# Kernel optimization log

Measured on AMD Instinct MI355X. Metric: run time of the kernel, lower is better.

The kernel has to match this reference:

```python
import jax, jax.numpy as jnp
import numpy as np

B, S, H = 8, 2048, 512
M = 4096
TEMP = 0.1
EPS = 1e-6


def setup_inputs() -> dict:
    key = jax.random.key(0)
    ks = jax.random.split(key, 8)
    scale = 1.0 / np.sqrt(H)
    return {
        "hidden_states": jax.random.normal(ks[0], (B, S, H), dtype=jnp.float32),
        "memory_keys": jax.random.normal(ks[1], (M, H), dtype=jnp.float32),
        "memory_values": jax.random.normal(ks[2], (M, H), dtype=jnp.float32),
        "Wk": jax.random.normal(ks[3], (H, H), dtype=jnp.float32) * scale,
        "bk": jnp.zeros((H,), dtype=jnp.float32),
        "Wo": jax.random.normal(ks[4], (H, H), dtype=jnp.float32) * scale,
        "bo": jnp.zeros((H,), dtype=jnp.float32),
        "memory_usage": jax.random.randint(ks[5], (M,), 0, 2, dtype=jnp.int32),
    }


def reference(hidden_states, memory_keys, memory_values, Wk, bk, Wo, bo, memory_usage):
    # key projection: [B,S,H]
    q = jnp.einsum("bsh,kh->bsk", hidden_states, Wk) + bk
    # L2-style normalization with eps inside rsqrt (matches torch.rsqrt(norm_sq + 1e-6))
    q_n = q * jax.lax.rsqrt(jnp.sum(q * q, axis=-1, keepdims=True) + EPS)
    mk_n = memory_keys * jax.lax.rsqrt(
        jnp.sum(memory_keys * memory_keys, axis=-1, keepdims=True) + EPS
    )
    # cosine-similarity scores over the memory bank: [B,S,M]
    scores = jnp.einsum("bsk,mk->bsm", q_n, mk_n) / TEMP
    mask = (memory_usage > 0).astype(scores.dtype)  # [M]
    scores = scores * mask + (-1e9) * (1.0 - mask)
    attn = jax.nn.softmax(scores, axis=-1)  # [B,S,M]
    retrieved = jnp.einsum("bsm,mv->bsv", attn, memory_values)  # [B,S,H]
    out = jnp.einsum("bsv,hv->bsh", retrieved, Wo) + bo
    return out
```

## Files before the change

### kernel.cpp

```cpp
#include <hip/hip_runtime.h>
#include <cstdint>
#include <cstddef>

#define H_DIM   512
#define M_DIM   4096

typedef unsigned short u16;
typedef short bf16x8 __attribute__((ext_vector_type(8)));
typedef float f32x4  __attribute__((ext_vector_type(4)));

__device__ __forceinline__ u16 f2b(float f) {
  union { float f; uint32_t u; } v; v.f = f;
  uint32_t u = v.u + (0x7FFFu + ((v.u >> 16) & 1u));
  return (u16)(u >> 16);
}

__global__ void k_f2bf(const float* __restrict__ in, u16* __restrict__ out, int n4) {
  int i = blockIdx.x * blockDim.x + threadIdx.x;
  if (i < n4) {
    float4 v = ((const float4*)in)[i];
    ushort4 o;
    o.x = f2b(v.x); o.y = f2b(v.y); o.z = f2b(v.z); o.w = f2b(v.w);
    ((ushort4*)out)[i] = o;
  }
}

__global__ void k_f2bf_ww(const float* __restrict__ wk, const float* __restrict__ wo,
                          u16* __restrict__ owk, u16* __restrict__ owo) {
  int i = blockIdx.x * blockDim.x + threadIdx.x;
  const float* src = (i < 65536) ? wk : wo;
  u16* dst = (i < 65536) ? owk : owo;
  int j = i & 65535;
  float4 v = ((const float4*)src)[j];
  ushort4 o;
  o.x = f2b(v.x); o.y = f2b(v.y); o.z = f2b(v.z); o.w = f2b(v.w);
  ((ushort4*)dst)[j] = o;
}

__global__ void k_compact(const int* __restrict__ usage, int* __restrict__ idx,
                          int* __restrict__ meta) {
  __shared__ int cnt[256];
  int t = threadIdx.x;
  int base = t * 16;
  int c = 0;
  #pragma unroll
  for (int i = 0; i < 16; ++i) c += (usage[base + i] > 0) ? 1 : 0;
  cnt[t] = c;
  __syncthreads();
  for (int d = 1; d < 256; d <<= 1) {
    int v = (t >= d) ? cnt[t - d] : 0;
    __syncthreads();
    cnt[t] += v;
    __syncthreads();
  }
  int pos = cnt[t] - c;
  for (int i = 0; i < 16; ++i)
    if (usage[base + i] > 0) idx[pos++] = base + i;
  if (t == 0) {
    int total = cnt[255];
    int keff = ((total + 127) >> 7) << 7;
    meta[0] = total; meta[1] = keff; meta[2] = keff >> 5; meta[3] = keff >> 7;
  }
}

__global__ void k_gather_both(const float* __restrict__ keys, const float* __restrict__ vals,
                              const int* __restrict__ idx, const int* __restrict__ meta,
                              u16* __restrict__ okeys, u16* __restrict__ ovals) {
  int j    = blockIdx.x * 4 + (threadIdx.x >> 6);
  int lane = threadIdx.x & 63;
  int count = meta[0];
  ushort4* kp = (ushort4*)(okeys + (size_t)j * H_DIM);
  ushort4* vp = (ushort4*)(ovals + (size_t)j * H_DIM);
  if (j >= count) {
    ushort4 z = {0, 0, 0, 0};
    kp[lane] = z; kp[lane + 64] = z;
    vp[lane] = z; vp[lane + 64] = z;
    return;
  }
  int src = idx[j];
  const float4* rp = (const float4*)(keys + (size_t)src * H_DIM);
  float4 a = rp[lane];
  float4 b = rp[lane + 64];
  float ss = a.x*a.x + a.y*a.y + a.z*a.z + a.w*a.w
           + b.x*b.x + b.y*b.y + b.z*b.z + b.w*b.w;
  #pragma unroll
  for (int d = 1; d < 64; d <<= 1) ss += __shfl_xor(ss, d, 64);
  float s = rsqrtf(ss + 1e-6f);
  ushort4 oa, ob;
  oa.x = f2b(a.x*s); oa.y = f2b(a.y*s); oa.z = f2b(a.z*s); oa.w = f2b(a.w*s);
  ob.x = f2b(b.x*s); ob.y = f2b(b.y*s); ob.z = f2b(b.z*s); ob.w = f2b(b.w*s);
  kp[lane]      = oa;
  kp[lane + 64] = ob;
  const float4* vr = (const float4*)(vals + (size_t)src * H_DIM);
  float4 c0 = vr[lane];
  float4 c1 = vr[lane + 64];
  ushort4 va, vb;
  va.x = f2b(c0.x); va.y = f2b(c0.y); va.z = f2b(c0.z); va.w = f2b(c0.w);
  vb.x = f2b(c1.x); vb.y = f2b(c1.y); vb.z = f2b(c1.z); vb.w = f2b(c1.w);
  vp[lane]      = va;
  vp[lane + 64] = vb;
}

__global__ void k_rsq(const float* __restrict__ qss, float* __restrict__ rsq) {
  int r = blockIdx.x * blockDim.x + threadIdx.x;
  float s = qss[r*4] + qss[r*4+1] + qss[r*4+2] + qss[r*4+3];
  rsq[r] = rsqrtf(s + 1e-6f);
}

__global__ void k_reduce_l(const float* __restrict__ lpart, float* __restrict__ linv,
                           const int* __restrict__ meta) {
  int r = blockIdx.x * blockDim.x + threadIdx.x;
  int n = meta[3];
  float s = 0.0f;
  for (int i = 0; i < n; ++i) s += lpart[(size_t)r * 32 + i];
  linv[r] = 1.0f / s;
}

#define EPI_QPROJ 0
#define EPI_MW    1
#define EPI_P     2
#define EPI_OUT   3

template<int EPI>
__global__ __launch_bounds__(256)
void k_gemm_bt(const u16* __restrict__ A, const u16* __restrict__ B,
               int N, int K,
               const int* __restrict__ meta,
               float* __restrict__ outf, u16* __restrict__ outh,
               const float* __restrict__ bias,
               float* __restrict__ aux,
               const float* __restrict__ rowscale) {
  __shared__ u16 Ah[2][128 * 32];
  __shared__ u16 Bh[2][128 * 32];
  __shared__ float lsh[128];

  const int tid  = threadIdx.x;
  const int wave = tid >> 6, lane = tid & 63;
  const int wr = (wave >> 1) * 64;
  const int wc = (wave & 1) * 64;

  int rb, cb0, cb_end, cb_step, kel;
  if (EPI == EPI_QPROJ) {
    rb = blockIdx.y; cb0 = blockIdx.x; cb_end = cb0 + 1; cb_step = 1; kel = K;
  } else if (EPI == EPI_MW) {
    rb = blockIdx.y; cb0 = blockIdx.x; cb_end = meta[1] >> 7; cb_step = 16; kel = K;
  } else if (EPI == EPI_P) {
    int id = blockIdx.x + (blockIdx.y << 4);
    int xcd = id & 7, s = id >> 3;
    rb = xcd * 16 + (s >> 4); cb0 = s & 15;
    cb_end = meta[1] >> 7; cb_step = 16; kel = K;
  } else {
    int id = blockIdx.x + (blockIdx.y << 2);
    int xcd = id & 7, s = id >> 3;
    rb = xcd * 16 + (s >> 2); cb0 = s & 3;
    cb_end = cb0 + 1; cb_step = 1; kel = meta[1];
  }
  const int row0 = rb << 7;
  const int kiters = kel >> 5;

  const int srow   = lane & 15;
  const int schunk = lane >> 4;
  const int lds_off = schunk * 128 + srow * 8;
  size_t aBase[2];
  #pragma unroll
  for (int s2 = 0; s2 < 2; ++s2)
    aBase[s2] = (size_t)(row0 + (wave + s2 * 4) * 16 + srow) * (size_t)K + schunk * 8;
  size_t bBase[2];

  const int fr = lane & 15;
  const int fbase = (lane >> 4) * 128 + fr * 8;

  for (int cb = cb0; cb < cb_end; cb += cb_step) {
    const int col0 = cb << 7;
    __syncthreads();
    if ((EPI == EPI_QPROJ || EPI == EPI_P) && tid < 128) lsh[tid] = 0.0f;

    #pragma unroll
    for (int s2 = 0; s2 < 2; ++s2)
      bBase[s2] = (size_t)(col0 + (wave + s2 * 4) * 16 + srow) * (size_t)K + schunk * 8;

    f32x4 acc[4][4];
    const f32x4 z = {0.0f, 0.0f, 0.0f, 0.0f};
    #pragma unroll
    for (int i = 0; i < 4; ++i)
      #pragma unroll
      for (int j = 0; j < 4; ++j) acc[i][j] = z;

    bf16x8 rA[2], rB[2];
    auto gload = [&](int k0) {
      #pragma unroll
      for (int s2 = 0; s2 < 2; ++s2) rA[s2] = *(const bf16x8*)(A + aBase[s2] + k0);
      #pragma unroll
      for (int s2 = 0; s2 < 2; ++s2) rB[s2] = *(const bf16x8*)(B + bBase[s2] + k0);
    };

    gload(0);
    for (int it = 0; it < kiters; ++it) {
      const int cur = it & 1;
      #pragma unroll
      for (int s2 = 0; s2 < 2; ++s2)
        *(bf16x8*)&Ah[cur][(wave + s2 * 4) * 512 + lds_off] = rA[s2];
      #pragma unroll
      for (int s2 = 0; s2 < 2; ++s2)
        *(bf16x8*)&Bh[cur][(wave + s2 * 4) * 512 + lds_off] = rB[s2];
      if (it + 1 < kiters) gload((it + 1) << 5);
      __syncthreads();

      bf16x8 af[4], bfv[4];
      #pragma unroll
      for (int i = 0; i < 4; ++i)
        af[i] = *(const bf16x8*)&Ah[cur][((wr >> 4) + i) * 512 + fbase];
      #pragma unroll
      for (int j = 0; j < 4; ++j)
        bfv[j] = *(const bf16x8*)&Bh[cur][((wc >> 4) + j) * 512 + fbase];
      #pragma unroll
      for (int i = 0; i < 4; ++i)
        #pragma unroll
        for (int j = 0; j < 4; ++j)
          acc[i][j] = __builtin_amdgcn_mfma_f32_16x16x32_bf16(af[i], bfv[j], acc[i][j], 0, 0, 0);
    }

    if (EPI == EPI_QPROJ) {
      float bv[4];
      #pragma unroll
      for (int j = 0; j < 4; ++j) bv[j] = bias[col0 + wc + j * 16 + fr];
      #pragma unroll
      for (int i = 0; i < 4; ++i) {
        #pragma unroll
        for (int r = 0; r < 4; ++r) {
          int lrow = wr + i * 16 + (lane >> 4) * 4 + r;
          size_t grow = (size_t)(row0 + lrow);
          float s = 0.0f;
          #pragma unroll
          for (int j = 0; j < 4; ++j) {
            int gcol = col0 + wc + j * 16 + fr;
            float v = acc[i][j][r] + bv[j];
            outh[grow * (size_t)N + gcol] = f2b(v);
            s += v * v;
          }
          #pragma unroll
          for (int d = 1; d < 16; d <<= 1) s += __shfl_xor(s, d, 64);
          if (fr == 0) atomicAdd(&lsh[lrow], s);
        }
      }
      __syncthreads();
      if (tid < 128) aux[(size_t)(row0 + tid) * 4 + cb] = lsh[tid];
    } else if (EPI == EPI_MW) {
      #pragma unroll
      for (int i = 0; i < 4; ++i) {
        #pragma unroll
        for (int r = 0; r < 4; ++r) {
          int grow = row0 + wr + i * 16 + (lane >> 4) * 4 + r;
          #pragma unroll
          for (int j = 0; j < 4; ++j) {
            int gcol = col0 + wc + j * 16 + fr;
            outh[(size_t)grow * (size_t)N + gcol] = f2b(acc[i][j][r]);
          }
        }
      }
    } else if (EPI == EPI_P) {
      const int count = meta[0];
      #pragma unroll
      for (int i = 0; i < 4; ++i) {
        #pragma unroll
        for (int r = 0; r < 4; ++r) {
          int lrow = wr + i * 16 + (lane >> 4) * 4 + r;
          size_t grow = (size_t)(row0 + lrow);
          float rq10 = rowscale[grow] * 10.0f;
          float s = 0.0f;
          #pragma unroll
          for (int j = 0; j < 4; ++j) {
            int gcol = col0 + wc + j * 16 + fr;
            float p = (gcol < count) ? __expf(acc[i][j][r] * rq10) : 0.0f;
            outh[grow * (size_t)N + gcol] = f2b(p);
            s += p;
          }
          #pragma unroll
          for (int d = 1; d < 16; d <<= 1) s += __shfl_xor(s, d, 64);
          if (fr == 0) atomicAdd(&lsh[lrow], s);
        }
      }
      __syncthreads();
      if (tid < 128) aux[(size_t)(row0 + tid) * 32 + cb] = lsh[tid];
    } else {
      float bv[4];
      #pragma unroll
      for (int j = 0; j < 4; ++j) bv[j] = bias[col0 + wc + j * 16 + fr];
      #pragma unroll
      for (int i = 0; i < 4; ++i) {
        #pragma unroll
        for (int r = 0; r < 4; ++r) {
          int grow = row0 + wr + i * 16 + (lane >> 4) * 4 + r;
          float sc = rowscale[grow];
          #pragma unroll
          for (int j = 0; j < 4; ++j) {
            int gcol = col0 + wc + j * 16 + fr;
            outf[(size_t)grow * (size_t)N + gcol] = acc[i][j][r] * sc + bv[j];
          }
        }
      }
    }
  }
}

extern "C" void kernel_launch(void* const* d_in, const int* in_sizes, int n_in,
                              void* d_out, int out_size, void* d_ws, size_t ws_size,
                              hipStream_t stream) {
  const float* hidden = (const float*)d_in[0];
  const float* mkeys  = (const float*)d_in[1];
  const float* mvals  = (const float*)d_in[2];
  const float* Wk     = (const float*)d_in[3];
  const float* bk     = (const float*)d_in[4];
  const float* Wo     = (const float*)d_in[5];
  const float* bo     = (const float*)d_in[6];
  const int*   usage  = (const int*)d_in[7];
  (void)in_sizes; (void)n_in; (void)out_size; (void)ws_size;

  char* ws = (char*)d_ws;
  u16*   hb    = (u16*)(ws + 0);
  int*   idx   = (int*)(ws + 0);
  int*   meta  = (int*)(ws + 16384);
  u16*   wkb   = (u16*)(ws + 16777216);
  u16*   wob   = (u16*)(ws + 17301504);
  u16*   mkn   = (u16*)(ws + 17825792);
  u16*   mv_c  = (u16*)(ws + 22020096);
  u16*   qb    = (u16*)(ws + 26214400);
  u16*   MWt   = (u16*)(ws + 42991616);
  u16*   P     = (u16*)(ws + 47185920);
  float* qss   = (float*)(ws + 181403648);
  float* rsqQ  = (float*)(ws + 181665792);
  float* lpart = (float*)(ws + 181731328);
  float* linv  = (float*)(ws + 183828480);

  k_f2bf<<<8192, 256, 0, stream>>>(hidden, hb, 2097152);
  k_f2bf_ww<<<512, 256, 0, stream>>>(Wk, Wo, wkb, wob);

  k_gemm_bt<EPI_QPROJ><<<dim3(4, 128), 256, 0, stream>>>(hb, wkb, 512, 512,
      nullptr, nullptr, qb, bk, qss, nullptr);
  k_rsq<<<64, 256, 0, stream>>>(qss, rsqQ);

  k_compact<<<1, 256, 0, stream>>>(usage, idx, meta);
  k_gather_both<<<1024, 256, 0, stream>>>(mkeys, mvals, idx, meta, mkn, mv_c);

  k_gemm_bt<EPI_MW><<<dim3(16, 4), 256, 0, stream>>>(wob, mv_c, M_DIM, 512,
      meta, nullptr, MWt, nullptr, nullptr, nullptr);

  k_gemm_bt<EPI_P><<<dim3(16, 128), 256, 0, stream>>>(qb, mkn, M_DIM, 512,
      meta, nullptr, P, nullptr, lpart, rsqQ);
  k_reduce_l<<<64, 256, 0, stream>>>(lpart, linv, meta);

  k_gemm_bt<EPI_OUT><<<dim3(4, 128), 256, 0, stream>>>(P, MWt, 512, M_DIM,
      meta, (float*)d_out, nullptr, bo, nullptr, linv);
}
```

Before: 292.1 us.

## Swap GEMM operands so epilogues write packed ushort4 along contiguous dim

The Q-projection and score GEMMs are restructured to compute the transposed tile (memory/weight rows as M, tokens as N), so each lane's four accumulator rows map to contiguous output elements and can be stored as one 8-byte ushort4 instead of scattered 2-byte stores. Row-sum partials for normalisation and softmax are now reduced with two shuffles and written straight to global memory, removing the LDS atomics and extra block barrier. The kernel also uses 32-bit byte offsets for global loads and raises the launch-bounds occupancy hint, and workspace buffers are relocated. The risk is extra register pressure from the occupancy hint and a larger partial-sum array to reduce afterwards.

```diff
diff --git a/kernel.cpp b/kernel.cpp
--- a/kernel.cpp
+++ b/kernel.cpp
@@ -103,16 +103,18 @@
 
 __global__ void k_rsq(const float* __restrict__ qss, float* __restrict__ rsq) {
   int r = blockIdx.x * blockDim.x + threadIdx.x;
-  float s = qss[r*4] + qss[r*4+1] + qss[r*4+2] + qss[r*4+3];
+  float s = 0.0f;
+  #pragma unroll
+  for (int i = 0; i < 8; ++i) s += qss[(size_t)r * 8 + i];
   rsq[r] = rsqrtf(s + 1e-6f);
 }
 
 __global__ void k_reduce_l(const float* __restrict__ lpart, float* __restrict__ linv,
                            const int* __restrict__ meta) {
   int r = blockIdx.x * blockDim.x + threadIdx.x;
-  int n = meta[3];
+  int n = meta[1] >> 6;
   float s = 0.0f;
-  for (int i = 0; i < n; ++i) s += lpart[(size_t)r * 32 + i];
+  for (int i = 0; i < n; ++i) s += lpart[(size_t)r * 64 + i];
   linv[r] = 1.0f / s;
 }
 
@@ -122,7 +124,7 @@
 #define EPI_OUT   3
 
 template<int EPI>
-__global__ __launch_bounds__(256)
+__global__ __launch_bounds__(256, 3)
 void k_gemm_bt(const u16* __restrict__ A, const u16* __restrict__ B,
                int N, int K,
                const int* __restrict__ meta,
@@ -132,52 +134,55 @@
                const float* __restrict__ rowscale) {
   __shared__ u16 Ah[2][128 * 32];
   __shared__ u16 Bh[2][128 * 32];
-  __shared__ float lsh[128];
 
   const int tid  = threadIdx.x;
   const int wave = tid >> 6, lane = tid & 63;
   const int wr = (wave >> 1) * 64;
   const int wc = (wave & 1) * 64;
 
-  int rb, cb0, cb_end, cb_step, kel;
+  int t0, t_end, t_step, kel, fixedb;
   if (EPI == EPI_QPROJ) {
-    rb = blockIdx.y; cb0 = blockIdx.x; cb_end = cb0 + 1; cb_step = 1; kel = K;
+    fixedb = blockIdx.x; t0 = blockIdx.y; t_end = t0 + 1; t_step = 1; kel = K;
   } else if (EPI == EPI_MW) {
-    rb = blockIdx.y; cb0 = blockIdx.x; cb_end = meta[1] >> 7; cb_step = 16; kel = K;
+    fixedb = blockIdx.y; t0 = blockIdx.x; t_end = meta[1] >> 7; t_step = 16; kel = K;
   } else if (EPI == EPI_P) {
     int id = blockIdx.x + (blockIdx.y << 4);
     int xcd = id & 7, s = id >> 3;
-    rb = xcd * 16 + (s >> 4); cb0 = s & 15;
-    cb_end = meta[1] >> 7; cb_step = 16; kel = K;
+    fixedb = xcd * 16 + (s >> 4);
+    t0 = s & 15;
+    t_end = meta[1] >> 7; t_step = 16; kel = K;
   } else {
     int id = blockIdx.x + (blockIdx.y << 2);
     int xcd = id & 7, s = id >> 3;
-    rb = xcd * 16 + (s >> 2); cb0 = s & 3;
-    cb_end = cb0 + 1; cb_step = 1; kel = meta[1];
-  }
-  const int row0 = rb << 7;
+    fixedb = xcd * 16 + (s >> 2);
+    t0 = s & 3; t_end = t0 + 1; t_step = 1; kel = meta[1];
+  }
   const int kiters = kel >> 5;
 
   const int srow   = lane & 15;
   const int schunk = lane >> 4;
   const int lds_off = schunk * 128 + srow * 8;
-  size_t aBase[2];
-  #pragma unroll
-  for (int s2 = 0; s2 < 2; ++s2)
-    aBase[s2] = (size_t)(row0 + (wave + s2 * 4) * 16 + srow) * (size_t)K + schunk * 8;
-  size_t bBase[2];
 
   const int fr = lane & 15;
   const int fbase = (lane >> 4) * 128 + fr * 8;
-
-  for (int cb = cb0; cb < cb_end; cb += cb_step) {
-    const int col0 = cb << 7;
+  const int g = lane >> 4;
+
+  const char* Ac = (const char*)A;
+  const char* Bc = (const char*)B;
+
+  for (int t = t0; t < t_end; t += t_step) {
+    const int row0 = ((EPI == EPI_P) ? t : fixedb) << 7;
+    const int col0 = ((EPI == EPI_P) ? fixedb : t) << 7;
     __syncthreads();
-    if ((EPI == EPI_QPROJ || EPI == EPI_P) && tid < 128) lsh[tid] = 0.0f;
-
+
+    uint32_t aB[2], bB[2];
     #pragma unroll
-    for (int s2 = 0; s2 < 2; ++s2)
-      bBase[s2] = (size_t)(col0 + (wave + s2 * 4) * 16 + srow) * (size_t)K + schunk * 8;
+    for (int s2 = 0; s2 < 2; ++s2) {
+      aB[s2] = (uint32_t)(((size_t)(row0 + (wave + s2 * 4) * 16 + srow) * (size_t)K
+                           + (size_t)(schunk * 8)) * 2u);
+      bB[s2] = (uint32_t)(((size_t)(col0 + (wave + s2 * 4) * 16 + srow) * (size_t)K
+                           + (size_t)(schunk * 8)) * 2u);
+    }
 
     f32x4 acc[4][4];
     const f32x4 z = {0.0f, 0.0f, 0.0f, 0.0f};
@@ -188,10 +193,11 @@
 
     bf16x8 rA[2], rB[2];
     auto gload = [&](int k0) {
-      #pragma unroll
-      for (int s2 = 0; s2 < 2; ++s2) rA[s2] = *(const bf16x8*)(A + aBase[s2] + k0);
-      #pragma unroll
-      for (int s2 = 0; s2 < 2; ++s2) rB[s2] = *(const bf16x8*)(B + bBase[s2] + k0);
+      const uint32_t kb = (uint32_t)(k0 << 1);
+      #pragma unroll
+      for (int s2 = 0; s2 < 2; ++s2) rA[s2] = *(const bf16x8*)(Ac + aB[s2] + kb);
+      #pragma unroll
+      for (int s2 = 0; s2 < 2; ++s2) rB[s2] = *(const bf16x8*)(Bc + bB[s2] + kb);
     };
 
     gload(0);
@@ -221,36 +227,38 @@
     }
 
     if (EPI == EPI_QPROJ) {
-      float bv[4];
-      #pragma unroll
-      for (int j = 0; j < 4; ++j) bv[j] = bias[col0 + wc + j * 16 + fr];
+      float sj[4] = {0.f, 0.f, 0.f, 0.f};
       #pragma unroll
       for (int i = 0; i < 4; ++i) {
+        const int kb = row0 + wr + i * 16 + g * 4;
+        const float4 bkv = *(const float4*)(bias + kb);
+        #pragma unroll
+        for (int j = 0; j < 4; ++j) {
+          const size_t rcol = (size_t)(col0 + wc + j * 16 + fr);
+          float v0 = acc[i][j][0] + bkv.x;
+          float v1 = acc[i][j][1] + bkv.y;
+          float v2 = acc[i][j][2] + bkv.z;
+          float v3 = acc[i][j][3] + bkv.w;
+          ushort4 st; st.x = f2b(v0); st.y = f2b(v1); st.z = f2b(v2); st.w = f2b(v3);
+          *(ushort4*)(outh + rcol * H_DIM + kb) = st;
+          sj[j] += v0 * v0 + v1 * v1 + v2 * v2 + v3 * v3;
+        }
+      }
+      const int slot = (row0 + wr) >> 6;
+      #pragma unroll
+      for (int j = 0; j < 4; ++j) {
+        float s = sj[j];
+        s += __shfl_xor(s, 16, 64);
+        s += __shfl_xor(s, 32, 64);
+        if (lane < 16)
+          aux[(size_t)(col0 + wc + j * 16 + lane) * 8 + slot] = s;
+      }
+    } else if (EPI == EPI_MW) {
+      #pragma unroll
+      for (int i = 0; i < 4; ++i) {
         #pragma unroll
         for (int r = 0; r < 4; ++r) {
-          int lrow = wr + i * 16 + (lane >> 4) * 4 + r;
-          size_t grow = (size_t)(row0 + lrow);
-          float s = 0.0f;
-          #pragma unroll
-          for (int j = 0; j < 4; ++j) {
-            int gcol = col0 + wc + j * 16 + fr;
-            float v = acc[i][j][r] + bv[j];
-            outh[grow * (size_t)N + gcol] = f2b(v);
-            s += v * v;
-          }
-          #pragma unroll
-          for (int d = 1; d < 16; d <<= 1) s += __shfl_xor(s, d, 64);
-          if (fr == 0) atomicAdd(&lsh[lrow], s);
-        }
-      }
-      __syncthreads();
-      if (tid < 128) aux[(size_t)(row0 + tid) * 4 + cb] = lsh[tid];
-    } else if (EPI == EPI_MW) {
-      #pragma unroll
-      for (int i = 0; i < 4; ++i) {
-        #pragma unroll
-        for (int r = 0; r < 4; ++r) {
-          int grow = row0 + wr + i * 16 + (lane >> 4) * 4 + r;
+          int grow = row0 + wr + i * 16 + g * 4 + r;
           #pragma unroll
           for (int j = 0; j < 4; ++j) {
             int gcol = col0 + wc + j * 16 + fr;
@@ -260,28 +268,35 @@
       }
     } else if (EPI == EPI_P) {
       const int count = meta[0];
+      float rq10[4];
+      #pragma unroll
+      for (int j = 0; j < 4; ++j)
+        rq10[j] = rowscale[col0 + wc + j * 16 + fr] * 10.0f;
+      float sj[4] = {0.f, 0.f, 0.f, 0.f};
       #pragma unroll
       for (int i = 0; i < 4; ++i) {
-        #pragma unroll
-        for (int r = 0; r < 4; ++r) {
-          int lrow = wr + i * 16 + (lane >> 4) * 4 + r;
-          size_t grow = (size_t)(row0 + lrow);
-          float rq10 = rowscale[grow] * 10.0f;
-          float s = 0.0f;
-          #pragma unroll
-          for (int j = 0; j < 4; ++j) {
-            int gcol = col0 + wc + j * 16 + fr;
-            float p = (gcol < count) ? __expf(acc[i][j][r] * rq10) : 0.0f;
-            outh[grow * (size_t)N + gcol] = f2b(p);
-            s += p;
-          }
-          #pragma unroll
-          for (int d = 1; d < 16; d <<= 1) s += __shfl_xor(s, d, 64);
-          if (fr == 0) atomicAdd(&lsh[lrow], s);
+        const int mb = row0 + wr + i * 16 + g * 4;
+        #pragma unroll
+        for (int j = 0; j < 4; ++j) {
+          const size_t rcol = (size_t)(col0 + wc + j * 16 + fr);
+          float p0 = (mb + 0 < count) ? __expf(acc[i][j][0] * rq10[j]) : 0.0f;
+          float p1 = (mb + 1 < count) ? __expf(acc[i][j][1] * rq10[j]) : 0.0f;
+          float p2 = (mb + 2 < count) ? __expf(acc[i][j][2] * rq10[j]) : 0.0f;
+          float p3 = (mb + 3 < count) ? __expf(acc[i][j][3] * rq10[j]) : 0.0f;
+          ushort4 st; st.x = f2b(p0); st.y = f2b(p1); st.z = f2b(p2); st.w = f2b(p3);
+          *(ushort4*)(outh + rcol * M_DIM + mb) = st;
+          sj[j] += (p0 + p1) + (p2 + p3);
         }
       }
-      __syncthreads();
-      if (tid < 128) aux[(size_t)(row0 + tid) * 32 + cb] = lsh[tid];
+      const int slot = (row0 + wr) >> 6;
+      #pragma unroll
+      for (int j = 0; j < 4; ++j) {
+        float s = sj[j];
+        s += __shfl_xor(s, 16, 64);
+        s += __shfl_xor(s, 32, 64);
+        if (lane < 16)
+          aux[(size_t)(col0 + wc + j * 16 + lane) * 64 + slot] = s;
+      }
     } else {
       float bv[4];
       #pragma unroll
@@ -290,7 +305,7 @@
       for (int i = 0; i < 4; ++i) {
         #pragma unroll
         for (int r = 0; r < 4; ++r) {
-          int grow = row0 + wr + i * 16 + (lane >> 4) * 4 + r;
+          int grow = row0 + wr + i * 16 + g * 4 + r;
           float sc = rowscale[grow];
           #pragma unroll
           for (int j = 0; j < 4; ++j) {
@@ -320,6 +335,7 @@
   u16*   hb    = (u16*)(ws + 0);
   int*   idx   = (int*)(ws + 0);
   int*   meta  = (int*)(ws + 16384);
+  float* lpart = (float*)(ws + 1048576);
   u16*   wkb   = (u16*)(ws + 16777216);
   u16*   wob   = (u16*)(ws + 17301504);
   u16*   mkn   = (u16*)(ws + 17825792);
@@ -327,15 +343,14 @@
   u16*   qb    = (u16*)(ws + 26214400);
   u16*   MWt   = (u16*)(ws + 42991616);
   u16*   P     = (u16*)(ws + 47185920);
-  float* qss   = (float*)(ws + 181403648);
+  float* qss   = (float*)(ws + 47185920);
   float* rsqQ  = (float*)(ws + 181665792);
-  float* lpart = (float*)(ws + 181731328);
   float* linv  = (float*)(ws + 183828480);
 
   k_f2bf<<<8192, 256, 0, stream>>>(hidden, hb, 2097152);
   k_f2bf_ww<<<512, 256, 0, stream>>>(Wk, Wo, wkb, wob);
 
-  k_gemm_bt<EPI_QPROJ><<<dim3(4, 128), 256, 0, stream>>>(hb, wkb, 512, 512,
+  k_gemm_bt<EPI_QPROJ><<<dim3(4, 128), 256, 0, stream>>>(wkb, hb, 512, 512,
       nullptr, nullptr, qb, bk, qss, nullptr);
   k_rsq<<<64, 256, 0, stream>>>(qss, rsqQ);
 
@@ -345,7 +360,7 @@
   k_gemm_bt<EPI_MW><<<dim3(16, 4), 256, 0, stream>>>(wob, mv_c, M_DIM, 512,
       meta, nullptr, MWt, nullptr, nullptr, nullptr);
 
-  k_gemm_bt<EPI_P><<<dim3(16, 128), 256, 0, stream>>>(qb, mkn, M_DIM, 512,
+  k_gemm_bt<EPI_P><<<dim3(16, 128), 256, 0, stream>>>(mkn, qb, M_DIM, 512,
       meta, nullptr, P, nullptr, lpart, rsqQ);
   k_reduce_l<<<64, 256, 0, stream>>>(lpart, linv, meta);
 
```

After: 292.4 us. No clear change (+0.1%).
